# Optimization experiments

Measured on AMD Instinct MI355X. Metric: run time of the kernel, lower is better.

Reference implementation:

```python
import jax, jax.numpy as jnp
import numpy as np

NUM_POINTS = 32
POINT_DIM = 4
HIDDEN_DIM = 256
BATCH = 8192


def setup_inputs() -> dict:
    key = jax.random.key(0)
    k1, k2, k3 = jax.random.split(key, 3)
    path_data = jax.random.normal(k1, (BATCH, NUM_POINTS * POINT_DIM), dtype=jnp.float32)
    # per-step Linear(point_dim+hidden_dim -> hidden_dim); torch Linear weight layout [out, in]
    fan_in = POINT_DIM + HIDDEN_DIM
    scale = 1.0 / np.sqrt(fan_in)
    W = jax.random.uniform(k2, (NUM_POINTS, HIDDEN_DIM, fan_in), dtype=jnp.float32, minval=-scale, maxval=scale)
    b = jax.random.uniform(k3, (NUM_POINTS, HIDDEN_DIM), dtype=jnp.float32, minval=-scale, maxval=scale)
    return {"path_data": path_data, "W": W, "b": b}


def reference(path_data, W, b):
    P, H = W.shape[0], W.shape[1]
    B = path_data.shape[0]
    pd = W.shape[2] - H
    # chunks: [P, B, point_dim]
    chunks = path_data.reshape(B, P, pd).transpose(1, 0, 2)

    def step(h, xs):
        wp, Wi, bi = xs
        # concat order matches torch: (curr_hidden, current_wp)
        combined = jnp.concatenate([h, wp], axis=1)  # [B, H+pd]
        h_new = jax.nn.relu(combined @ Wi.T + bi)    # [B, H]
        return h_new, h_new

    h0 = jnp.zeros((B, H), dtype=path_data.dtype)
    _, feats = jax.lax.scan(step, h0, (chunks, W, b))  # feats: [P, B, H]
    return feats.transpose(1, 0, 2).reshape(B, P * H)
```

## Files before the change

kernel.cpp:

```cpp
#include <hip/hip_runtime.h>

typedef __attribute__((ext_vector_type(8))) short bf16x8;
typedef __attribute__((ext_vector_type(16))) float f32x16;

#define NPTS 32
#define HID 256
#define FANIN 260
#define NKB 17
#define OUTSTRIDE 8192

__device__ __forceinline__ unsigned short f2bf(float f) {
  unsigned u = __builtin_bit_cast(unsigned, f);
  u += 0x7fffu + ((u >> 16) & 1u);
  return (unsigned short)(u >> 16);
}

__global__ __launch_bounds__(256) void prep_kernel(
    const float* __restrict__ W, const float* __restrict__ bias,
    bf16x8* __restrict__ pack) {
  int tid = blockIdx.x * 256 + threadIdx.x;
  int lane = tid & 63;
  int kb = (tid >> 6) % NKB;
  int rest = (tid >> 6) / NKB;
  int ct = rest & 7;
  int p = rest >> 3;
  if (p >= NPTS) return;
  int n = ct * 32 + (lane & 31);
  int g = lane >> 5;
  const float* wrow = W + (size_t)(p * HID + n) * FANIN;
  unsigned short e[8];
  if (kb < 16) {
    int k0 = kb * 16 + g * 8;
#pragma unroll
    for (int i = 0; i < 8; ++i) e[i] = f2bf(wrow[k0 + i]);
  } else {
#pragma unroll
    for (int i = 0; i < 8; ++i) e[i] = 0;
    if (g == 0) {
      e[0] = f2bf(wrow[256]);
      e[1] = f2bf(wrow[257]);
      e[2] = f2bf(wrow[258]);
      e[3] = f2bf(wrow[259]);
      e[4] = f2bf(bias[p * HID + n]);
    }
  }
  bf16x8 v;
#pragma unroll
  for (int i = 0; i < 8; ++i) v[i] = (short)e[i];
  pack[tid] = v;
}

__global__ __launch_bounds__(512, 2) void enc_kernel(
    const float* __restrict__ path, const bf16x8* __restrict__ pack,
    float* __restrict__ out) {
  __shared__ __align__(16) char lds[32768];
  const int tid = threadIdx.x;
  const int lane = tid & 63;
  const int w = tid >> 6;
  const int col = lane & 31;
  const int g = lane >> 5;
  const int b0 = blockIdx.x * 32;

  {
    int4 z = make_int4(0, 0, 0, 0);
    *reinterpret_cast<int4*>(lds + tid * 32) = z;
    *reinterpret_cast<int4*>(lds + tid * 32 + 16) = z;
  }

  const float4* prow =
      reinterpret_cast<const float4*>(path + (size_t)(b0 + col) * 128);
  float* outbase = out + (size_t)b0 * OUTSTRIDE;
  const int swz = col << 4;
  int cur = 0;

  bf16x8 BA[NKB], BB[NKB];
  float4 pxA, pxB;
  {
    const bf16x8* Bp0 = pack + (size_t)w * NKB * 64 + lane;
#pragma unroll
    for (int kb = 0; kb < NKB; ++kb) BA[kb] = Bp0[kb * 64];
    pxA = prow[0];
  }
  __syncthreads();

#define STEP(P, BC, BN, PX, PXN, PNEXT)                                       \
  {                                                                           \
    const int p_ = (P);                                                       \
    const bf16x8* Bnp =                                                       \
        pack + ((size_t)((PNEXT) * 8 + w) * NKB) * 64 + lane;                 \
    f32x16 acc0, acc1;                                                        \
    _Pragma("unroll") for (int i = 0; i < 16; ++i) {                          \
      acc0[i] = 0.0f;                                                         \
      acc1[i] = 0.0f;                                                         \
    }                                                                         \
    bf16x8 ax;                                                                \
    _Pragma("unroll") for (int i = 0; i < 8; ++i) ax[i] = 0;                  \
    if (g == 0) {                                                             \
      ax[0] = (short)f2bf((PX).x);                                            \
      ax[1] = (short)f2bf((PX).y);                                            \
      ax[2] = (short)f2bf((PX).z);                                            \
      ax[3] = (short)f2bf((PX).w);                                            \
      ax[4] = (short)0x3F80;                \
    }                                                                         \
    const char* hb = lds + cur * 16384;                                       \
    _Pragma("unroll") for (int kb = 0; kb < 16; ++kb) {                       \
      bf16x8 a = *reinterpret_cast<const bf16x8*>(                            \
          hb + col * 512 + ((kb * 32 + g * 16) ^ swz));                       \
      if (kb & 1)                                                             \
        acc1 = __builtin_amdgcn_mfma_f32_32x32x16_bf16(a, (BC)[kb], acc1,     \
                                                       0, 0, 0);              \
      else                                                                    \
        acc0 = __builtin_amdgcn_mfma_f32_32x32x16_bf16(a, (BC)[kb], acc0,     \
                                                       0, 0, 0);              \
      (BN)[kb] = Bnp[kb * 64]; \
    }                                                                         \
    acc0 = __builtin_amdgcn_mfma_f32_32x32x16_bf16(ax, (BC)[16], acc0,        \
                                                   0, 0, 0);                  \
    (BN)[16] = Bnp[16 * 64];                                                  \
    (PXN) = prow[(PNEXT)];                                                    \
    char* hn = lds + (cur ^ 1) * 16384;                                       \
    float* outp = outbase + p_ * 256 + w * 32 + col;                          \
    _Pragma("unroll") for (int r = 0; r < 16; ++r) {                          \
      int rr = (r & 3) + 8 * (r >> 2) + 4 * g;        \
      float v = fmaxf(acc0[r] + acc1[r], 0.0f);                               \
      __builtin_nontemporal_store(v, outp + (size_t)rr * OUTSTRIDE);          \
      *reinterpret_cast<unsigned short*>(                                     \
          hn + rr * 512 + (((w * 32 + col) * 2) ^ (rr << 4))) = f2bf(v);      \
    }                                                                         \
    asm volatile("s_waitcnt lgkmcnt(0)" ::: "memory");                        \
    __builtin_amdgcn_s_barrier();                                             \
    cur ^= 1;                                                                 \
  }

  for (int p = 0; p < NPTS; p += 2) {
    const int pn2 = (p + 2 < NPTS) ? (p + 2) : 0;
    STEP(p, BA, BB, pxA, pxB, (p + 1));
    STEP((p + 1), BB, BA, pxB, pxA, pn2);
  }
#undef STEP
}

extern "C" void kernel_launch(void* const* d_in, const int* in_sizes, int n_in,
                              void* d_out, int out_size, void* d_ws,
                              size_t ws_size, hipStream_t stream) {
  const float* path = (const float*)d_in[0];
  const float* W = (const float*)d_in[1];
  const float* bias = (const float*)d_in[2];
  float* out = (float*)d_out;
  bf16x8* pack = (bf16x8*)d_ws;

  prep_kernel<<<1088, 256, 0, stream>>>(W, bias, pack);
  enc_kernel<<<256, 512, 0, stream>>>(path, pack, out);
}
```

Before: 93.54 us.

## Stage weight tiles through LDS in prep and rotate wave column assignment

The prep kernel now loads a contiguous 32-row weight tile per block into shared memory with vectorized loads, then converts to bf16 from LDS. Previously each thread read eight strided floats straight from global memory. The encoder also rotates which 32-column output tile each wave owns by block index. This spreads concurrent weight-pack reads and output stores across different addresses instead of every block hitting the same ones. The costs are a large 33KB LDS buffer in prep, which limits its occupancy, and fewer prep blocks.

```diff
diff --git a/kernel.cpp b/kernel.cpp
--- a/kernel.cpp
+++ b/kernel.cpp
@@ -2,6 +2,7 @@
 
 typedef __attribute__((ext_vector_type(8))) short bf16x8;
 typedef __attribute__((ext_vector_type(16))) float f32x16;
+typedef __attribute__((ext_vector_type(4))) float f32x4;
 
 #define NPTS 32
 #define HID 256
@@ -18,36 +19,40 @@
 __global__ __launch_bounds__(256) void prep_kernel(
     const float* __restrict__ W, const float* __restrict__ bias,
     bf16x8* __restrict__ pack) {
-  int tid = blockIdx.x * 256 + threadIdx.x;
-  int lane = tid & 63;
-  int kb = (tid >> 6) % NKB;
-  int rest = (tid >> 6) / NKB;
-  int ct = rest & 7;
-  int p = rest >> 3;
-  if (p >= NPTS) return;
-  int n = ct * 32 + (lane & 31);
-  int g = lane >> 5;
-  const float* wrow = W + (size_t)(p * HID + n) * FANIN;
-  unsigned short e[8];
-  if (kb < 16) {
-    int k0 = kb * 16 + g * 8;
-#pragma unroll
-    for (int i = 0; i < 8; ++i) e[i] = f2bf(wrow[k0 + i]);
-  } else {
+  __shared__ float wl[32 * FANIN];
+  const int p = blockIdx.x >> 3;
+  const int nb = blockIdx.x & 7;
+  const int t = threadIdx.x;
+  const f32x4* src = reinterpret_cast<const f32x4*>(
+      W + ((size_t)p * HID + nb * 32) * FANIN);
+  for (int i = t; i < 32 * FANIN / 4; i += 256)
+    *reinterpret_cast<f32x4*>(wl + i * 4) = src[i];
+  __syncthreads();
+  const int lane = t & 63;
+  const int wv = t >> 6;
+  const int m = lane & 31;
+  const int g = lane >> 5;
+  const float* rowp = wl + m * FANIN;
+  for (int kb = wv; kb < NKB; kb += 4) {
+    unsigned short e[8];
 #pragma unroll
     for (int i = 0; i < 8; ++i) e[i] = 0;
-    if (g == 0) {
-      e[0] = f2bf(wrow[256]);
-      e[1] = f2bf(wrow[257]);
-      e[2] = f2bf(wrow[258]);
-      e[3] = f2bf(wrow[259]);
-      e[4] = f2bf(bias[p * HID + n]);
+    if (kb < 16) {
+      int k0 = kb * 16 + g * 8;
+#pragma unroll
+      for (int i = 0; i < 8; ++i) e[i] = f2bf(rowp[k0 + i]);
+    } else if (g == 0) {
+      e[0] = f2bf(rowp[256]);
+      e[1] = f2bf(rowp[257]);
+      e[2] = f2bf(rowp[258]);
+      e[3] = f2bf(rowp[259]);
+      e[4] = f2bf(bias[p * HID + nb * 32 + m]);
     }
+    bf16x8 v;
+#pragma unroll
+    for (int i = 0; i < 8; ++i) v[i] = (short)e[i];
+    pack[(((size_t)p * 8 + nb) * NKB + kb) * 64 + lane] = v;
   }
-  bf16x8 v;
-#pragma unroll
-  for (int i = 0; i < 8; ++i) v[i] = (short)e[i];
-  pack[tid] = v;
 }
 
 __global__ __launch_bounds__(512, 2) void enc_kernel(
@@ -57,14 +62,15 @@
   const int tid = threadIdx.x;
   const int lane = tid & 63;
   const int w = tid >> 6;
+  const int t = (w + (int)blockIdx.x) & 7;
   const int col = lane & 31;
   const int g = lane >> 5;
   const int b0 = blockIdx.x * 32;
 
   {
-    int4 z = make_int4(0, 0, 0, 0);
-    *reinterpret_cast<int4*>(lds + tid * 32) = z;
-    *reinterpret_cast<int4*>(lds + tid * 32 + 16) = z;
+    f32x4 z = {0.0f, 0.0f, 0.0f, 0.0f};
+    *reinterpret_cast<f32x4*>(lds + tid * 32) = z;
+    *reinterpret_cast<f32x4*>(lds + tid * 32 + 16) = z;
   }
 
   const float4* prow =
@@ -76,7 +82,7 @@
   bf16x8 BA[NKB], BB[NKB];
   float4 pxA, pxB;
   {
-    const bf16x8* Bp0 = pack + (size_t)w * NKB * 64 + lane;
+    const bf16x8* Bp0 = pack + (size_t)t * NKB * 64 + lane;
 #pragma unroll
     for (int kb = 0; kb < NKB; ++kb) BA[kb] = Bp0[kb * 64];
     pxA = prow[0];
@@ -87,7 +93,7 @@
   {                                                                           \
     const int p_ = (P);                                                       \
     const bf16x8* Bnp =                                                       \
-        pack + ((size_t)((PNEXT) * 8 + w) * NKB) * 64 + lane;                 \
+        pack + ((size_t)((PNEXT) * 8 + t) * NKB) * 64 + lane;                 \
     f32x16 acc0, acc1;                                                        \
     _Pragma("unroll") for (int i = 0; i < 16; ++i) {                          \
       acc0[i] = 0.0f;                                                         \
@@ -112,20 +118,20 @@
       else                                                                    \
         acc0 = __builtin_amdgcn_mfma_f32_32x32x16_bf16(a, (BC)[kb], acc0,     \
                                                        0, 0, 0);              \
-      (BN)[kb] = Bnp[kb * 64]; \
+      (BN)[kb] = Bnp[kb * 64];       \
     }                                                                         \
     acc0 = __builtin_amdgcn_mfma_f32_32x32x16_bf16(ax, (BC)[16], acc0,        \
                                                    0, 0, 0);                  \
     (BN)[16] = Bnp[16 * 64];                                                  \
     (PXN) = prow[(PNEXT)];                                                    \
     char* hn = lds + (cur ^ 1) * 16384;                                       \
-    float* outp = outbase + p_ * 256 + w * 32 + col;                          \
+    float* outp = outbase + p_ * 256 + t * 32 + col;                          \
     _Pragma("unroll") for (int r = 0; r < 16; ++r) {                          \
       int rr = (r & 3) + 8 * (r >> 2) + 4 * g;        \
       float v = fmaxf(acc0[r] + acc1[r], 0.0f);                               \
       __builtin_nontemporal_store(v, outp + (size_t)rr * OUTSTRIDE);          \
       *reinterpret_cast<unsigned short*>(                                     \
-          hn + rr * 512 + (((w * 32 + col) * 2) ^ (rr << 4))) = f2bf(v);      \
+          hn + rr * 512 + (((t * 32 + col) * 2) ^ (rr << 4))) = f2bf(v);      \
     }                                                                         \
     asm volatile("s_waitcnt lgkmcnt(0)" ::: "memory");                        \
     __builtin_amdgcn_s_barrier();                                             \
@@ -149,6 +155,6 @@
   float* out = (float*)d_out;
   bf16x8* pack = (bf16x8*)d_ws;
 
-  prep_kernel<<<1088, 256, 0, stream>>>(W, bias, pack);
+  prep_kernel<<<256, 256, 0, stream>>>(W, bias, pack);
   enc_kernel<<<256, 512, 0, stream>>>(path, pack, out);
 }
```

Result: slower. 95.88 us (+2.5%).
